# Optimization experiments

Measured on AMD Instinct MI355X. Metric: run time of the kernel, lower is better.

The kernel has to match this reference:

```python
import jax, jax.numpy as jnp
import numpy as np

VOCAB = 50257
EMB = 512
HID = 256
NCLS = 20
PAD = 0


def setup_inputs() -> dict:
    key = jax.random.key(0)
    ks = jax.random.split(key, 10)
    s_e = 1.0 / np.sqrt(EMB)
    s_h = 1.0 / np.sqrt(HID)
    x = jax.random.randint(ks[0], (32, 2048), 0, VOCAB, dtype=jnp.int64)
    return {
        "x": x,
        "emb": jax.random.normal(ks[1], (VOCAB, EMB), jnp.float32),
        "w_ih": jax.random.uniform(ks[2], (4 * HID, EMB), jnp.float32, -s_h, s_h),
        "w_hh": jax.random.uniform(ks[3], (4 * HID, HID), jnp.float32, -s_h, s_h),
        "b_ih": jax.random.uniform(ks[4], (4 * HID,), jnp.float32, -s_h, s_h),
        "b_hh": jax.random.uniform(ks[5], (4 * HID,), jnp.float32, -s_h, s_h),
        "w1": jax.random.uniform(ks[6], (2 * HID, HID), jnp.float32, -s_h, s_h),
        "b1": jax.random.uniform(ks[7], (2 * HID,), jnp.float32, -s_h, s_h),
        "w2": jax.random.uniform(ks[8], (NCLS, 2 * HID), jnp.float32, -1.0 / np.sqrt(2 * HID), 1.0 / np.sqrt(2 * HID)),
        "b2": jax.random.uniform(ks[9], (NCLS,), jnp.float32, -1.0 / np.sqrt(2 * HID), 1.0 / np.sqrt(2 * HID)),
    }


def _lstm(xe, w_ih, w_hh, b_ih, b_hh):
    # xe: (B, T, E) -> hs: (B, T, H). PyTorch gate order: i, f, g, o.
    B, T, E = xe.shape
    H = w_hh.shape[1]
    # Precompute input contribution for all timesteps (one big GEMM).
    xg = jnp.einsum('bte,ge->btg', xe, w_ih) + b_ih + b_hh  # (B, T, 4H)
    xg = jnp.swapaxes(xg, 0, 1)  # (T, B, 4H)

    def step(carry, xt):
        h, c = carry
        gates = xt + h @ w_hh.T  # (B, 4H)
        i, f, g, o = jnp.split(gates, 4, axis=-1)
        i = jax.nn.sigmoid(i)
        f = jax.nn.sigmoid(f)
        g = jnp.tanh(g)
        o = jax.nn.sigmoid(o)
        c = f * c + i * g
        h = o * jnp.tanh(c)
        return (h, c), h

    h0 = jnp.zeros((B, H), xe.dtype)
    c0 = jnp.zeros((B, H), xe.dtype)
    _, hs = jax.lax.scan(step, (h0, c0), xg)
    return jnp.swapaxes(hs, 0, 1)  # (B, T, H)


def reference(x, emb, w_ih, w_hh, b_ih, b_hh, w1, b1, w2, b2):
    mask = (x != PAD)  # (B, T)
    lens = mask.sum(axis=1)  # (B,)
    xe = emb[x]  # (B, T, E)
    h = _lstm(xe, w_ih, w_hh, b_ih, b_hh)  # (B, T, H)
    pooled = (h * mask[:, :, None]).sum(axis=1) / lens[:, None].astype(h.dtype)
    # dropout omitted (inference / eval mode)
    lin1 = jax.nn.relu(pooled @ w1.T + b1)
    return lin1 @ w2.T + b2  # (B, n_classes)
```

## Files before the change

### kernel.cpp

```cpp
#include <hip/hip_runtime.h>
#include <hip/hip_fp16.h>

typedef _Float16 f16;
typedef _Float16 f16x2 __attribute__((ext_vector_type(2)));
typedef _Float16 f16x8 __attribute__((ext_vector_type(8)));
typedef float f32x4 __attribute__((ext_vector_type(4)));

#define B_    32
#define T_    2048
#define E_    512
#define H_    256
#define G4_   1024
#define VOCAB_ 50257

static const size_t WS_XG   = 0;
static const size_t WS_WIH  = 134217728ull;
static const size_t WS_WREG = 135266304ull;
static const size_t WS_WLDS = 135659520ull;
static const size_t WS_BSUM = 135790592ull;
static const size_t WS_POOL = 135794688ull;
static const size_t WS_LENS = 135827456ull;

#define HB_OFF 131072
#define LDS_BYTES (131072 + 1088)

__device__ __forceinline__ unsigned pack2f(float a, float b) {
    f16x2 h; h.x = (f16)a; h.y = (f16)b;
    return __builtin_bit_cast(unsigned, h);
}

__device__ __forceinline__ float fdot2u(unsigned a, unsigned b, float c) {
#if __has_builtin(__builtin_amdgcn_fdot2)
    return __builtin_amdgcn_fdot2(__builtin_bit_cast(f16x2, a),
                                  __builtin_bit_cast(f16x2, b), c, false);
#else
    f16x2 av = __builtin_bit_cast(f16x2, a), bv = __builtin_bit_cast(f16x2, b);
    return c + (float)av.x * (float)bv.x + (float)av.y * (float)bv.y;
#endif
}

__device__ __forceinline__ float sigm(float v) {
    return 1.f / (1.f + exp2f(-1.44269504f * v));
}
__device__ __forceinline__ float tanhr(float v) {
    float t = exp2f(-2.88539008f * fabsf(v));
    float r = (1.f - t) / (1.f + t);
    return v < 0.f ? -r : r;
}

__device__ __forceinline__ int detect64(const int* x) {
    return (x[1] == 0 && x[3] == 0 && x[5] == 0) ? 1 : 0;
}

__global__ void prep_k(const float* __restrict__ w_ih, const float* __restrict__ w_hh,
                       const float* __restrict__ b_ih, const float* __restrict__ b_hh,
                       f16* __restrict__ wih16, unsigned* __restrict__ wreg,
                       uint4* __restrict__ wlds, float* __restrict__ bsum)
{
    const int gid = blockIdx.x * blockDim.x + threadIdx.x;
    const int stride = gridDim.x * blockDim.x;
    for (int i = gid; i < G4_*E_; i += stride) wih16[i] = (f16)w_ih[i];
    for (int i = gid; i < G4_; i += stride) bsum[i] = b_ih[i] + b_hh[i];
    for (int n = gid; n < 192*512; n += stride) {
        const int ii = n >> 9, t = n & 511;
        const int wv = t >> 6, lane = t & 63, kc = lane & 1, li = lane >> 1;
        const int j = wv*32 + li;
        const int q = ii / 48, rem = ii % 48, cc = rem >> 2, u = rem & 3;
        const int row = q*256 + j;
        const int k = kc*128 + cc*8 + u*2;
        wreg[n] = pack2f(w_hh[row*256 + k], w_hh[row*256 + k + 1]);
    }
    for (int m = gid; m < 8*16*64; m += stride) {
        const int lane = m & 63, s = (m >> 6) & 15, wv = m >> 10;
        const int kc = lane & 1, li = lane >> 1;
        const int j = wv*32 + li;
        const int q = s >> 2, e = s & 3;
        const int row = q*256 + j;
        const int kb = kc*128 + 96 + e*8;
        uint4 v;
        v.x = pack2f(w_hh[row*256 + kb + 0], w_hh[row*256 + kb + 1]);
        v.y = pack2f(w_hh[row*256 + kb + 2], w_hh[row*256 + kb + 3]);
        v.z = pack2f(w_hh[row*256 + kb + 4], w_hh[row*256 + kb + 5]);
        v.w = pack2f(w_hh[row*256 + kb + 6], w_hh[row*256 + kb + 7]);
        wlds[m] = v;
    }
}

__global__ __launch_bounds__(256) void gemm_xg_k(
    const int* __restrict__ x, const float* __restrict__ emb,
    const f16* __restrict__ wih, const float* __restrict__ bsum,
    f16* __restrict__ xg)
{
    __shared__ f16 As[128*32];
    __shared__ f16 Bs[128*32];
    const int tid = threadIdx.x;
    const int bid = blockIdx.x;
    const int mt = bid >> 3, nt = bid & 7;
    const int wv = tid >> 6, lane = tid & 63;
    const int wm = wv & 1, wn = wv >> 1;
    const int ml = lane & 15, kg = lane >> 4;
    const int is64 = detect64(x);
    const int r = tid >> 1, kh = tid & 1;
    int tok = x[(mt*128 + r) << is64];
    tok = tok < 0 ? 0 : (tok >= VOCAB_ ? VOCAB_ - 1 : tok);
    const float* arow = emb + (size_t)tok * E_ + kh*16;
    const f16*   brow = wih + (size_t)(nt*128 + r) * E_ + kh*16;

    f32x4 acc[4][4] = {};
    for (int kk = 0; kk < 16; ++kk) {
        const int k0 = kk * 32;
        float4 a0 = *(const float4*)(arow + k0 + 0);
        float4 a1 = *(const float4*)(arow + k0 + 4);
        float4 a2 = *(const float4*)(arow + k0 + 8);
        float4 a3 = *(const float4*)(arow + k0 + 12);
        uint4 bu0 = *(const uint4*)(brow + k0);
        uint4 bu1 = *(const uint4*)(brow + k0 + 8);
        uint4 au0, au1;
        au0.x = pack2f(a0.x, a0.y); au0.y = pack2f(a0.z, a0.w);
        au0.z = pack2f(a1.x, a1.y); au0.w = pack2f(a1.z, a1.w);
        au1.x = pack2f(a2.x, a2.y); au1.y = pack2f(a2.z, a2.w);
        au1.z = pack2f(a3.x, a3.y); au1.w = pack2f(a3.z, a3.w);
        __syncthreads();
        *(uint4*)(&As[r*32 + kh*16 + 0]) = au0;
        *(uint4*)(&As[r*32 + kh*16 + 8]) = au1;
        *(uint4*)(&Bs[r*32 + kh*16 + 0]) = bu0;
        *(uint4*)(&Bs[r*32 + kh*16 + 8]) = bu1;
        __syncthreads();
        f16x8 af[4], bf[4];
        #pragma unroll
        for (int i = 0; i < 4; ++i) {
            af[i] = *(const f16x8*)(&As[(wm*64 + i*16 + ml)*32 + kg*8]);
            bf[i] = *(const f16x8*)(&Bs[(wn*64 + i*16 + ml)*32 + kg*8]);
        }
        #pragma unroll
        for (int i = 0; i < 4; ++i)
            #pragma unroll
            for (int j = 0; j < 4; ++j)
                acc[i][j] = __builtin_amdgcn_mfma_f32_16x16x32_f16(af[i], bf[j], acc[i][j], 0, 0, 0);
    }
    #pragma unroll
    for (int j = 0; j < 4; ++j) {
        const int gc = nt*128 + wn*64 + j*16 + ml;
        const float bs = bsum[gc];
        const int pc = ((gc & 255) << 2) | (gc >> 8);
        #pragma unroll
        for (int i = 0; i < 4; ++i) {
            #pragma unroll
            for (int q = 0; q < 4; ++q) {
                const int gr = mt*128 + wm*64 + i*16 + kg*4 + q;
                xg[(size_t)gr*G4_ + pc] = (f16)(acc[i][j][q] + bs);
            }
        }
    }
}

__global__ __attribute__((amdgpu_flat_work_group_size(512, 512), amdgpu_waves_per_eu(2, 2)))
void recur_k(
    const int* __restrict__ x, const f16* __restrict__ xg,
    const unsigned* __restrict__ wreg_g, const uint4* __restrict__ wlds_g,
    float* __restrict__ pool, float* __restrict__ lens)
{
    extern __shared__ char smem[];
    const int tid = threadIdx.x, b = blockIdx.x;
    const int wv = tid >> 6, lane = tid & 63, kc = lane & 1, li = lane >> 1;
    const int j = wv*32 + li;
    const int is64 = detect64(x);

    unsigned wr[192];
    #pragma unroll
    for (int i = 0; i < 192; ++i) wr[i] = wreg_g[i*512 + tid];
    #pragma unroll
    for (int i = 0; i < 192; ++i) asm volatile("" : "+v"(wr[i]));
    {
        uint4* wl = (uint4*)smem;
        #pragma unroll
        for (int s = 0; s < 16; ++s)
            wl[wv*1024 + s*64 + lane] = wlds_g[wv*1024 + s*64 + lane];
    }
    if (tid < 272) ((unsigned*)(smem + HB_OFF))[tid] = 0u;

    const int* xrow = x + (((size_t)b * T_) << is64);
    const char* xgrow = (const char*)xg + (size_t)b * T_ * 2048;
    const char* wbase = smem + wv*16384;
    float cst = 0.f, pooled = 0.f; int len = 0;
    __syncthreads();

    for (int t = 0; t < T_; ++t) {
        const char* hb = smem + HB_OFF + (t & 1)*544 + kc*272;
        uint2 xv = *(const uint2*)(xgrow + (size_t)t*2048 + j*8);
        const int tokm = xrow[(size_t)t << is64];
        float p[4] = {0.f, 0.f, 0.f, 0.f};
        #pragma unroll
        for (int cc = 0; cc < 12; ++cc) {
            uint4 hp = *(const uint4*)(hb + cc*16);
            #pragma unroll
            for (int q = 0; q < 4; ++q) {
                p[q] = fdot2u(wr[q*48 + cc*4 + 0], hp.x, p[q]);
                p[q] = fdot2u(wr[q*48 + cc*4 + 1], hp.y, p[q]);
                p[q] = fdot2u(wr[q*48 + cc*4 + 2], hp.z, p[q]);
                p[q] = fdot2u(wr[q*48 + cc*4 + 3], hp.w, p[q]);
            }
        }
        #pragma unroll
        for (int e = 0; e < 4; ++e) {
            uint4 hp = *(const uint4*)(hb + 192 + e*16);
            #pragma unroll
            for (int q = 0; q < 4; ++q) {
                uint4 w4 = *(const uint4*)(wbase + ((q*4 + e)*64 + lane)*16);
                p[q] = fdot2u(w4.x, hp.x, p[q]);
                p[q] = fdot2u(w4.y, hp.y, p[q]);
                p[q] = fdot2u(w4.z, hp.z, p[q]);
                p[q] = fdot2u(w4.w, hp.w, p[q]);
            }
        }
        #pragma unroll
        for (int q = 0; q < 4; ++q) p[q] += __shfl_xor(p[q], 1);

        f16x2 x01 = __builtin_bit_cast(f16x2, xv.x);
        f16x2 x23 = __builtin_bit_cast(f16x2, xv.y);
        float ai = sigm (p[0] + (float)x01.x);
        float af = sigm (p[1] + (float)x01.y);
        float ag = tanhr(p[2] + (float)x23.x);
        float ao = sigm (p[3] + (float)x23.y);
        cst = af*cst + ai*ag;
        float hv = ao * tanhr(cst);
        if (kc == 0) {
            *(f16*)(smem + HB_OFF + ((t+1) & 1)*544 + (j >> 7)*272 + (j & 127)*2) = (f16)hv;
            if (tokm != 0) { pooled += hv; ++len; }
        }
        __syncthreads();
    }
    if (kc == 0) pool[b*H_ + j] = pooled;
    if (tid == 0) lens[b] = (float)len;
}

__global__ __launch_bounds__(256) void head_k(
    const float* __restrict__ pool, const float* __restrict__ lens,
    const float* __restrict__ w1, const float* __restrict__ b1,
    const float* __restrict__ w2, const float* __restrict__ b2,
    float* __restrict__ out)
{
    __shared__ float pl[256];
    __shared__ float l1[512];
    const int b = blockIdx.x, tid = threadIdx.x;
    const float inv = 1.f / lens[b];
    pl[tid] = pool[b*256 + tid] * inv;
    __syncthreads();
    for (int o = tid; o < 512; o += 256) {
        const float4* wrow = (const float4*)(w1 + (size_t)o*256);
        float s = b1[o];
        #pragma unroll 8
        for (int k = 0; k < 64; ++k) {
            float4 wv = wrow[k];
            s += pl[k*4+0]*wv.x + pl[k*4+1]*wv.y + pl[k*4+2]*wv.z + pl[k*4+3]*wv.w;
        }
        l1[o] = fmaxf(s, 0.f);
    }
    __syncthreads();
    if (tid < 20) {
        const float4* wrow = (const float4*)(w2 + (size_t)tid*512);
        float s = b2[tid];
        #pragma unroll 8
        for (int k = 0; k < 128; ++k) {
            float4 wv = wrow[k];
            s += l1[k*4+0]*wv.x + l1[k*4+1]*wv.y + l1[k*4+2]*wv.z + l1[k*4+3]*wv.w;
        }
        out[b*20 + tid] = s;
    }
}

extern "C" void kernel_launch(void* const* d_in, const int* in_sizes, int n_in,
                              void* d_out, int out_size, void* d_ws, size_t ws_size,
                              hipStream_t stream) {
    (void)in_sizes; (void)n_in; (void)out_size; (void)ws_size;
    const int*   x    = (const int*)d_in[0];
    const float* emb  = (const float*)d_in[1];
    const float* w_ih = (const float*)d_in[2];
    const float* w_hh = (const float*)d_in[3];
    const float* b_ih = (const float*)d_in[4];
    const float* b_hh = (const float*)d_in[5];
    const float* w1   = (const float*)d_in[6];
    const float* b1   = (const float*)d_in[7];
    const float* w2   = (const float*)d_in[8];
    const float* b2   = (const float*)d_in[9];
    float* out = (float*)d_out;
    char* ws = (char*)d_ws;

    f16*      xg    = (f16*)(ws + WS_XG);
    f16*      wih16 = (f16*)(ws + WS_WIH);
    unsigned* wreg  = (unsigned*)(ws + WS_WREG);
    uint4*    wlds  = (uint4*)(ws + WS_WLDS);
    float*    bsum  = (float*)(ws + WS_BSUM);
    float*    pool  = (float*)(ws + WS_POOL);
    float*    lensb = (float*)(ws + WS_LENS);

    hipLaunchKernelGGL(prep_k, dim3(512), dim3(256), 0, stream,
                       w_ih, w_hh, b_ih, b_hh, wih16, wreg, wlds, bsum);
    hipLaunchKernelGGL(gemm_xg_k, dim3(4096), dim3(256), 0, stream,
                       x, emb, wih16, bsum, xg);
    hipLaunchKernelGGL(recur_k, dim3(32), dim3(512), LDS_BYTES, stream,
                       x, xg, wreg, wlds, pool, lensb);
    hipLaunchKernelGGL(head_k, dim3(32), dim3(256), 0, stream,
                       pool, lensb, w1, b1, w2, b2, out);
}
```

Baseline: 3.745 ms.

## Split LSTM recurrence K-halves across waves with readlane broadcast and LDS partial sums

Each hidden unit's dot product is now split across two waves (by K half) rather than across adjacent lanes. The h vector is loaded once per lane and broadcast through readlane into scalar registers instead of repeated LDS vector reads. Partial sums are exchanged through LDS, which adds a second barrier per timestep, and only one wave of each pair computes the gate nonlinearities. The per-timestep token mask is precomputed as a bitmask in prep, and the length count moves to the head kernel.

```diff
diff --git a/kernel.cpp b/kernel.cpp
--- a/kernel.cpp
+++ b/kernel.cpp
@@ -17,12 +17,11 @@
 static const size_t WS_WIH  = 134217728ull;
 static const size_t WS_WREG = 135266304ull;
 static const size_t WS_WLDS = 135659520ull;
-static const size_t WS_BSUM = 135790592ull;
-static const size_t WS_POOL = 135794688ull;
-static const size_t WS_LENS = 135827456ull;
-
-#define HB_OFF 131072
-#define LDS_BYTES (131072 + 1088)
+static const size_t WS_MB   = 135790592ull;
+static const size_t WS_BSUM = 135798784ull;
+static const size_t WS_POOL = 135802880ull;
+
+#define LDS_BYTES 140288
 
 __device__ __forceinline__ unsigned pack2f(float a, float b) {
     f16x2 h; h.x = (f16)a; h.y = (f16)b;
@@ -52,37 +51,52 @@
     return (x[1] == 0 && x[3] == 0 && x[5] == 0) ? 1 : 0;
 }
 
-__global__ void prep_k(const float* __restrict__ w_ih, const float* __restrict__ w_hh,
+__global__ void prep_k(const int* __restrict__ x,
+                       const float* __restrict__ w_ih, const float* __restrict__ w_hh,
                        const float* __restrict__ b_ih, const float* __restrict__ b_hh,
                        f16* __restrict__ wih16, unsigned* __restrict__ wreg,
-                       uint4* __restrict__ wlds, float* __restrict__ bsum)
+                       uint4* __restrict__ wlds, unsigned* __restrict__ mb,
+                       float* __restrict__ bsum)
 {
     const int gid = blockIdx.x * blockDim.x + threadIdx.x;
     const int stride = gridDim.x * blockDim.x;
+    const int is64 = detect64(x);
     for (int i = gid; i < G4_*E_; i += stride) wih16[i] = (f16)w_ih[i];
     for (int i = gid; i < G4_; i += stride) bsum[i] = b_ih[i] + b_hh[i];
     for (int n = gid; n < 192*512; n += stride) {
-        const int ii = n >> 9, t = n & 511;
-        const int wv = t >> 6, lane = t & 63, kc = lane & 1, li = lane >> 1;
-        const int j = wv*32 + li;
-        const int q = ii / 48, rem = ii % 48, cc = rem >> 2, u = rem & 3;
+        const int idx = n >> 9, tid = n & 511;
+        const int wv = tid >> 6, lane = tid & 63, kc = wv & 1, jg = wv >> 1;
+        const int j = jg*64 + lane;
+        const int q = idx / 48, m = idx % 48;
         const int row = q*256 + j;
-        const int k = kc*128 + cc*8 + u*2;
-        wreg[n] = pack2f(w_hh[row*256 + k], w_hh[row*256 + k + 1]);
-    }
-    for (int m = gid; m < 8*16*64; m += stride) {
-        const int lane = m & 63, s = (m >> 6) & 15, wv = m >> 10;
-        const int kc = lane & 1, li = lane >> 1;
-        const int j = wv*32 + li;
+        const int k0 = kc*128 + (m >> 1)*4 + (m & 1)*2;
+        wreg[n] = pack2f(w_hh[row*256 + k0], w_hh[row*256 + k0 + 1]);
+    }
+    for (int n = gid; n < 8*16*64; n += stride) {
+        const int lane = n & 63, s = (n >> 6) & 15, wv = n >> 10;
+        const int kc = wv & 1, jg = wv >> 1;
+        const int j = jg*64 + lane;
         const int q = s >> 2, e = s & 3;
         const int row = q*256 + j;
-        const int kb = kc*128 + 96 + e*8;
-        uint4 v;
-        v.x = pack2f(w_hh[row*256 + kb + 0], w_hh[row*256 + kb + 1]);
-        v.y = pack2f(w_hh[row*256 + kb + 2], w_hh[row*256 + kb + 3]);
-        v.z = pack2f(w_hh[row*256 + kb + 4], w_hh[row*256 + kb + 5]);
-        v.w = pack2f(w_hh[row*256 + kb + 6], w_hh[row*256 + kb + 7]);
-        wlds[m] = v;
+        const float* wrow = w_hh + (size_t)row*H_;
+        uint4 v; unsigned d[4];
+        #pragma unroll
+        for (int u = 0; u < 4; ++u) {
+            const int m = 48 + 4*e + u;
+            const int k0 = kc*128 + (m >> 1)*4 + (m & 1)*2;
+            d[u] = pack2f(wrow[k0], wrow[k0 + 1]);
+        }
+        v.x = d[0]; v.y = d[1]; v.z = d[2]; v.w = d[3];
+        wlds[n] = v;
+    }
+    for (int i = gid; i < 32*64; i += stride) {
+        const int b = i >> 6, wd = i & 63;
+        unsigned word = 0;
+        for (int tt = 0; tt < 32; ++tt) {
+            const size_t ti = ((size_t)b*T_ + wd*32 + tt) << is64;
+            word |= (x[ti] != 0 ? 1u : 0u) << tt;
+        }
+        mb[i] = word;
     }
 }
 
@@ -101,7 +115,7 @@
     const int ml = lane & 15, kg = lane >> 4;
     const int is64 = detect64(x);
     const int r = tid >> 1, kh = tid & 1;
-    int tok = x[(mt*128 + r) << is64];
+    int tok = x[(size_t)(mt*128 + r) << is64];
     tok = tok < 0 ? 0 : (tok >= VOCAB_ ? VOCAB_ - 1 : tok);
     const float* arow = emb + (size_t)tok * E_ + kh*16;
     const f16*   brow = wih + (size_t)(nt*128 + r) * E_ + kh*16;
@@ -155,16 +169,17 @@
 }
 
 __global__ __attribute__((amdgpu_flat_work_group_size(512, 512), amdgpu_waves_per_eu(2, 2)))
-void recur_k(
-    const int* __restrict__ x, const f16* __restrict__ xg,
-    const unsigned* __restrict__ wreg_g, const uint4* __restrict__ wlds_g,
-    float* __restrict__ pool, float* __restrict__ lens)
+void recur_k(const f16* __restrict__ xg,
+             const unsigned* __restrict__ wreg_g, const uint4* __restrict__ wlds_g,
+             const unsigned* __restrict__ mb,
+             float* __restrict__ pool)
 {
     extern __shared__ char smem[];
     const int tid = threadIdx.x, b = blockIdx.x;
-    const int wv = tid >> 6, lane = tid & 63, kc = lane & 1, li = lane >> 1;
-    const int j = wv*32 + li;
-    const int is64 = detect64(x);
+    const int wv = tid >> 6, lane = tid & 63;
+    const int kc = wv & 1, jg = wv >> 1;
+    const int j = jg*64 + lane;
+    const int kcb = kc*32;
 
     unsigned wr[192];
     #pragma unroll
@@ -177,73 +192,106 @@
         for (int s = 0; s < 16; ++s)
             wl[wv*1024 + s*64 + lane] = wlds_g[wv*1024 + s*64 + lane];
     }
-    if (tid < 272) ((unsigned*)(smem + HB_OFF))[tid] = 0u;
-
-    const int* xrow = x + (((size_t)b * T_) << is64);
+    if (tid < 256) ((unsigned*)(smem + 131072))[tid] = 0u;
+
     const char* xgrow = (const char*)xg + (size_t)b * T_ * 2048;
     const char* wbase = smem + wv*16384;
-    float cst = 0.f, pooled = 0.f; int len = 0;
+    char* pbuf = smem + 132096;
+    float cst = 0.f, pooled = 0.f;
+    unsigned mw = 0;
     __syncthreads();
 
     for (int t = 0; t < T_; ++t) {
-        const char* hb = smem + HB_OFF + (t & 1)*544 + kc*272;
-        uint2 xv = *(const uint2*)(xgrow + (size_t)t*2048 + j*8);
-        const int tokm = xrow[(size_t)t << is64];
+        const char* hb = smem + 131072 + (t & 1)*512;
+        uint2 hv = *(const uint2*)(hb + lane*8);
+        uint2 xv = {0, 0};
+        if (kc == 0) {
+            xv = *(const uint2*)(xgrow + (size_t)t*2048 + j*8);
+            if ((t & 31) == 0) mw = mb[b*64 + (t >> 5)];
+        }
         float p[4] = {0.f, 0.f, 0.f, 0.f};
-        #pragma unroll
-        for (int cc = 0; cc < 12; ++cc) {
-            uint4 hp = *(const uint4*)(hb + cc*16);
-            #pragma unroll
-            for (int q = 0; q < 4; ++q) {
-                p[q] = fdot2u(wr[q*48 + cc*4 + 0], hp.x, p[q]);
-                p[q] = fdot2u(wr[q*48 + cc*4 + 1], hp.y, p[q]);
-                p[q] = fdot2u(wr[q*48 + cc*4 + 2], hp.z, p[q]);
-                p[q] = fdot2u(wr[q*48 + cc*4 + 3], hp.w, p[q]);
-            }
-        }
-        #pragma unroll
-        for (int e = 0; e < 4; ++e) {
-            uint4 hp = *(const uint4*)(hb + 192 + e*16);
-            #pragma unroll
-            for (int q = 0; q < 4; ++q) {
-                uint4 w4 = *(const uint4*)(wbase + ((q*4 + e)*64 + lane)*16);
-                p[q] = fdot2u(w4.x, hp.x, p[q]);
-                p[q] = fdot2u(w4.y, hp.y, p[q]);
-                p[q] = fdot2u(w4.z, hp.z, p[q]);
-                p[q] = fdot2u(w4.w, hp.w, p[q]);
-            }
-        }
-        #pragma unroll
-        for (int q = 0; q < 4; ++q) p[q] += __shfl_xor(p[q], 1);
-
-        f16x2 x01 = __builtin_bit_cast(f16x2, xv.x);
-        f16x2 x23 = __builtin_bit_cast(f16x2, xv.y);
-        float ai = sigm (p[0] + (float)x01.x);
-        float af = sigm (p[1] + (float)x01.y);
-        float ag = tanhr(p[2] + (float)x23.x);
-        float ao = sigm (p[3] + (float)x23.y);
-        cst = af*cst + ai*ag;
-        float hv = ao * tanhr(cst);
+
+        {
+            unsigned sA[16], sB[16];
+            #pragma unroll
+            for (int i = 0; i < 16; ++i) {
+                sA[i] = __builtin_amdgcn_readlane((int)hv.x, kcb + i);
+                sB[i] = __builtin_amdgcn_readlane((int)hv.y, kcb + i);
+            }
+            #pragma unroll
+            for (int m = 0; m < 32; ++m) {
+                const unsigned h2 = (m & 1) ? sB[m >> 1] : sA[m >> 1];
+                #pragma unroll
+                for (int q = 0; q < 4; ++q) p[q] = fdot2u(wr[q*48 + m], h2, p[q]);
+            }
+        }
+        {
+            unsigned sA[16], sB[16];
+            #pragma unroll
+            for (int i = 0; i < 16; ++i) {
+                sA[i] = __builtin_amdgcn_readlane((int)hv.x, kcb + 16 + i);
+                sB[i] = __builtin_amdgcn_readlane((int)hv.y, kcb + 16 + i);
+            }
+            #pragma unroll
+            for (int m = 32; m < 48; ++m) {
+                const unsigned h2 = (m & 1) ? sB[(m >> 1) - 16] : sA[(m >> 1) - 16];
+                #pragma unroll
+                for (int q = 0; q < 4; ++q) p[q] = fdot2u(wr[q*48 + m], h2, p[q]);
+            }
+            #pragma unroll
+            for (int e = 0; e < 4; ++e) {
+                const unsigned hA0 = sA[8 + 2*e], hB0 = sB[8 + 2*e];
+                const unsigned hA1 = sA[9 + 2*e], hB1 = sB[9 + 2*e];
+                #pragma unroll
+                for (int q = 0; q < 4; ++q) {
+                    uint4 w4 = *(const uint4*)(wbase + ((q*4 + e)*64 + lane)*16);
+                    p[q] = fdot2u(w4.x, hA0, p[q]);
+                    p[q] = fdot2u(w4.y, hB0, p[q]);
+                    p[q] = fdot2u(w4.z, hA1, p[q]);
+                    p[q] = fdot2u(w4.w, hB1, p[q]);
+                }
+            }
+        }
+        *(float4*)(pbuf + wv*1024 + lane*16) = make_float4(p[0], p[1], p[2], p[3]);
+        __syncthreads();
         if (kc == 0) {
-            *(f16*)(smem + HB_OFF + ((t+1) & 1)*544 + (j >> 7)*272 + (j & 127)*2) = (f16)hv;
-            if (tokm != 0) { pooled += hv; ++len; }
+            float4 pr = *(const float4*)(pbuf + (wv^1)*1024 + lane*16);
+            f16x2 x01 = __builtin_bit_cast(f16x2, xv.x);
+            f16x2 x23 = __builtin_bit_cast(f16x2, xv.y);
+            float gi = sigm (p[0] + pr.x + (float)x01.x);
+            float gf = sigm (p[1] + pr.y + (float)x01.y);
+            float gg = tanhr(p[2] + pr.z + (float)x23.x);
+            float go = sigm (p[3] + pr.w + (float)x23.y);
+            cst = gf*cst + gi*gg;
+            float hvv = go * tanhr(cst);
+            if ((mw >> (t & 31)) & 1) pooled += hvv;
+            *(f16*)(smem + 131072 + ((t+1) & 1)*512 + j*2) = (f16)hvv;
         }
         __syncthreads();
     }
     if (kc == 0) pool[b*H_ + j] = pooled;
-    if (tid == 0) lens[b] = (float)len;
 }
 
 __global__ __launch_bounds__(256) void head_k(
-    const float* __restrict__ pool, const float* __restrict__ lens,
+    const int* __restrict__ x,
+    const float* __restrict__ pool,
     const float* __restrict__ w1, const float* __restrict__ b1,
     const float* __restrict__ w2, const float* __restrict__ b2,
     float* __restrict__ out)
 {
     __shared__ float pl[256];
     __shared__ float l1[512];
+    __shared__ int wcnt[4];
     const int b = blockIdx.x, tid = threadIdx.x;
-    const float inv = 1.f / lens[b];
+    const int is64 = detect64(x);
+    const int* xrow = x + (((size_t)b * T_) << is64);
+    int cnt = 0;
+    for (int k = tid; k < T_; k += 256) cnt += (xrow[(size_t)k << is64] != 0);
+    #pragma unroll
+    for (int s = 32; s > 0; s >>= 1) cnt += __shfl_xor(cnt, s);
+    if ((tid & 63) == 0) wcnt[tid >> 6] = cnt;
+    __syncthreads();
+    const float inv = 1.f / (float)(wcnt[0] + wcnt[1] + wcnt[2] + wcnt[3]);
     pl[tid] = pool[b*256 + tid] * inv;
     __syncthreads();
     for (int o = tid; o < 512; o += 256) {
@@ -290,16 +338,16 @@
     f16*      wih16 = (f16*)(ws + WS_WIH);
     unsigned* wreg  = (unsigned*)(ws + WS_WREG);
     uint4*    wlds  = (uint4*)(ws + WS_WLDS);
+    unsigned* mb    = (unsigned*)(ws + WS_MB);
     float*    bsum  = (float*)(ws + WS_BSUM);
     float*    pool  = (float*)(ws + WS_POOL);
-    float*    lensb = (float*)(ws + WS_LENS);
 
     hipLaunchKernelGGL(prep_k, dim3(512), dim3(256), 0, stream,
-                       w_ih, w_hh, b_ih, b_hh, wih16, wreg, wlds, bsum);
+                       x, w_ih, w_hh, b_ih, b_hh, wih16, wreg, wlds, mb, bsum);
     hipLaunchKernelGGL(gemm_xg_k, dim3(4096), dim3(256), 0, stream,
                        x, emb, wih16, bsum, xg);
     hipLaunchKernelGGL(recur_k, dim3(32), dim3(512), LDS_BYTES, stream,
-                       x, xg, wreg, wlds, pool, lensb);
+                       xg, wreg, wlds, mb, pool);
     hipLaunchKernelGGL(head_k, dim3(32), dim3(256), 0, stream,
-                       pool, lensb, w1, b1, w2, b2, out);
-}
+                       x, pool, w1, b1, w2, b2, out);
+}
```

After: 5.248 ms. 1.4x slower.
